# Kernel tuning notes

Hardware: AMD Instinct MI355X
Metric: run time of the kernel (lower is better)

## Reference

```python
import math
import jax, jax.numpy as jnp
import numpy as np

B, N, HID, NH = 4, 1024, 1024, 16
DH = HID // NH
MLP = int(HID * 4.0)


def _ndense(x, w):
    # NormalizedDense: row-normalize kernel (axis=1 for 2D), alpha=sqrt(w[0].size)=sqrt(out),
    # then divide by sqrt(fan_in).
    norm = jnp.linalg.norm(w, axis=1, keepdims=True)
    alpha = jnp.sqrt(jnp.asarray(w.shape[1], x.dtype))
    wn = w / (norm * alpha + 1e-4)
    wn = wn / jnp.sqrt(jnp.asarray(w.shape[0], x.dtype))
    return x @ wn


def mp_silu(x):
    return jax.nn.silu(x) / 0.596


def pixel_norm(x, eps=1e-4):
    return x * jax.lax.rsqrt(jnp.mean(x * x, axis=-1, keepdims=True) + eps)


def mp_add(a, b, t=0.3):
    return ((1 - t) * a + t * b) / math.sqrt((1 - t) ** 2 + t ** 2)


def setup_inputs() -> dict:
    key = jax.random.key(0)
    ks = jax.random.split(key, 9)
    std = 0.02
    return {
        "x": jax.random.normal(ks[0], (B, N, HID), jnp.float32),
        "c": jax.random.normal(ks[1], (B, HID), jnp.float32),
        "w_cond": std * jax.random.normal(ks[2], (HID, 2 * HID), jnp.float32),
        "w_qkv": std * jax.random.normal(ks[3], (HID, 3 * HID), jnp.float32),
        "w_out": std * jax.random.normal(ks[4], (HID, HID), jnp.float32),
        "w_mlp1": std * jax.random.normal(ks[5], (HID, MLP), jnp.float32),
        "w_mlp2": std * jax.random.normal(ks[6], (MLP, HID), jnp.float32),
        "attn_gain": 0.1 * jax.random.normal(ks[7], (), jnp.float32),
        "mlp_gain": 0.1 * jax.random.normal(ks[8], (), jnp.float32),
    }


def reference(x, c, w_cond, w_qkv, w_out, w_mlp1, w_mlp2, attn_gain, mlp_gain):
    # conditioning -> gain/shift
    cc = mp_silu(c)
    cc = _ndense(cc, w_cond)                       # [B, 2H]
    gain, shift = jnp.split(cc, 2, axis=-1)        # [B, H] each

    # attention branch
    x_cond = pixel_norm(x) * (1 + gain[:, None]) + shift[:, None]
    qkv = _ndense(x_cond, w_qkv)                   # [B, N, 3H]
    q, k, v = jnp.split(qkv, 3, axis=-1)
    q, k, v = pixel_norm(q), pixel_norm(k), pixel_norm(v)

    def split_heads(t):
        return t.reshape(B, N, NH, DH).transpose(0, 2, 1, 3)  # [B, NH, N, DH]

    q, k, v = split_heads(q), split_heads(k), split_heads(v)
    q = q / jnp.sqrt(jnp.sum(q * q, axis=-1, keepdims=True) + 1e-6)
    k = k / jnp.sqrt(jnp.sum(k * k, axis=-1, keepdims=True) + 1e-6)

    attn = jnp.einsum('bhnd,bhmd->bhnm', q, k) / math.sqrt(DH)
    attn = jax.nn.softmax(attn, axis=-1)
    x_attn = jnp.einsum('bhnm,bhmd->bhnd', attn, v)
    x_attn = x_attn.transpose(0, 2, 1, 3).reshape(B, N, HID)
    x_attn = pixel_norm(_ndense(x_attn, w_out)) * jnp.exp(attn_gain)
    x = mp_add(x, x_attn, t=0.3)

    # MLP branch
    x_cond = pixel_norm(x) * (1 + gain[:, None]) + shift[:, None]
    h = mp_silu(pixel_norm(_ndense(x_cond, w_mlp1)))
    x_mlp = pixel_norm(_ndense(h, w_mlp2)) * jnp.exp(mlp_gain)
    x = mp_add(x, x_mlp, t=0.3)
    return x
```

## Files before the change

### kernel.cpp

```cpp
#include <hip/hip_runtime.h>

typedef __bf16 bf16_t;
typedef __attribute__((ext_vector_type(8))) __bf16 bh8;
typedef __attribute__((ext_vector_type(4))) __bf16 bh4;
typedef __attribute__((ext_vector_type(4))) float f32x4;

#define DEV static __device__ __forceinline__

typedef __attribute__((address_space(3))) void lds_void;
typedef const __attribute__((address_space(1))) void glb_void;

DEV void async16(const bf16_t* g, bf16_t* l) {
  __builtin_amdgcn_global_load_lds((glb_void*)g, (lds_void*)l, 16, 0, 0);
}

DEV float wave_sum(float v) {
#pragma unroll
  for (int m = 32; m > 0; m >>= 1) v += __shfl_xor(v, m, 64);
  return v;
}

DEV float block_sum(float v, float* sbuf) {
  v = wave_sum(v);
  int wid = threadIdx.x >> 6;
  if ((threadIdx.x & 63) == 0) sbuf[wid] = v;
  __syncthreads();
  float r = sbuf[0] + sbuf[1] + sbuf[2] + sbuf[3];
  __syncthreads();
  return r;
}

__global__ void k_wnorm_all(const float* __restrict__ w_cond, const float* __restrict__ w_qkv,
                            const float* __restrict__ w_out, const float* __restrict__ w_mlp1,
                            const float* __restrict__ w_mlp2, float* __restrict__ s) {
  __shared__ float sbuf[4];
  int id = blockIdx.x;
  const float* W; int N, K, row;
  if (id < 1024)      { W = w_cond; N = 2048; K = 1024; row = id; }
  else if (id < 2048) { W = w_qkv;  N = 3072; K = 1024; row = id - 1024; }
  else if (id < 3072) { W = w_out;  N = 1024; K = 1024; row = id - 2048; }
  else if (id < 4096) { W = w_mlp1; N = 4096; K = 1024; row = id - 3072; }
  else                { W = w_mlp2; N = 1024; K = 4096; row = id - 4096; }
  const float4* wr = (const float4*)(W + (size_t)row * N);
  float acc = 0.f;
  for (int i = threadIdx.x; i < (N >> 2); i += 256) {
    float4 w = wr[i];
    acc += w.x*w.x + w.y*w.y + w.z*w.z + w.w*w.w;
  }
  float tot = block_sum(acc, sbuf);
  if (threadIdx.x == 0) {
    float norm = sqrtf(tot);
    s[id] = 1.0f / ((norm * sqrtf((float)N) + 1e-4f) * sqrtf((float)K));
  }
}

__global__ void k_wtrans_all(const float* __restrict__ w_cond, const float* __restrict__ w_qkv,
                             const float* __restrict__ w_out, const float* __restrict__ w_mlp1,
                             const float* __restrict__ w_mlp2, const float* __restrict__ sall,
                             bf16_t* __restrict__ wt_cond, bf16_t* __restrict__ wt_qkv,
                             bf16_t* __restrict__ wt_out, bf16_t* __restrict__ wt_mlp1,
                             bf16_t* __restrict__ wt_mlp2) {
  __shared__ float tile[64][65];
  int id = blockIdx.x;
  const float* W; const float* s; bf16_t* Wt; int K, N, n0, k0;
  if (id < 512)       { W=w_cond; s=sall;      Wt=wt_cond; K=1024; N=2048; int l=id;      n0=(l&31)*64; k0=(l>>5)*64; }
  else if (id < 1280) { W=w_qkv;  s=sall+1024; Wt=wt_qkv;  K=1024; N=3072; int l=id-512;  n0=(l%48)*64; k0=(l/48)*64; }
  else if (id < 1536) { W=w_out;  s=sall+2048; Wt=wt_out;  K=1024; N=1024; int l=id-1280; n0=(l&15)*64; k0=(l>>4)*64; }
  else if (id < 2560) { W=w_mlp1; s=sall+3072; Wt=wt_mlp1; K=1024; N=4096; int l=id-1536; n0=(l&63)*64; k0=(l>>6)*64; }
  else                { W=w_mlp2; s=sall+4096; Wt=wt_mlp2; K=4096; N=1024; int l=id-2560; n0=(l&15)*64; k0=(l>>4)*64; }
  int tx = threadIdx.x & 63, ty = threadIdx.x >> 6;
  for (int r = ty; r < 64; r += 4)
    tile[r][tx] = W[(size_t)(k0 + r) * N + n0 + tx] * s[k0 + r];
  __syncthreads();
  for (int r = ty; r < 64; r += 4)
    Wt[(size_t)(n0 + r) * K + k0 + tx] = (bf16_t)tile[tx][r];
}

__global__ void k_cond(const float* __restrict__ c, const bf16_t* __restrict__ wt,
                       float* __restrict__ gs) {
  __shared__ float cc[4][1024];
  int t = threadIdx.x;
  for (int i = t; i < 4096; i += 256) {
    int b = i >> 10, col = i & 1023;
    float x = c[b * 1024 + col];
    float sig = 1.f / (1.f + __expf(-x));
    cc[b][col] = x * sig * (1.f / 0.596f);
  }
  __syncthreads();
  int wid = t >> 6, lane = t & 63;
  int j = blockIdx.x * 4 + wid;
  const bf16_t* wr = wt + (size_t)j * 1024;
  float acc0 = 0, acc1 = 0, acc2 = 0, acc3 = 0;
  for (int i = lane; i < 1024; i += 64) {
    float w = (float)wr[i];
    acc0 += cc[0][i] * w; acc1 += cc[1][i] * w;
    acc2 += cc[2][i] * w; acc3 += cc[3][i] * w;
  }
  float v0 = wave_sum(acc0), v1 = wave_sum(acc1), v2 = wave_sum(acc2), v3 = wave_sum(acc3);
  if (lane == 0) {
    gs[0 * 2048 + j] = v0; gs[1 * 2048 + j] = v1;
    gs[2 * 2048 + j] = v2; gs[3 * 2048 + j] = v3;
  }
}

__global__ void k_xcond(const float* __restrict__ x, const float* __restrict__ gs,
                        bf16_t* __restrict__ xc) {
  __shared__ float sbuf[4];
  int row = blockIdx.x, b = row >> 10, t = threadIdx.x;
  float4 v = ((const float4*)(x + (size_t)row * 1024))[t];
  float ss = v.x*v.x + v.y*v.y + v.z*v.z + v.w*v.w;
  float tot = block_sum(ss, sbuf);
  float r = rsqrtf(tot * (1.f/1024.f) + 1e-4f);
  float4 g  = ((const float4*)(gs + b * 2048))[t];
  float4 sh = ((const float4*)(gs + b * 2048 + 1024))[t];
  bh4 o;
  o[0] = (bf16_t)(v.x * r * (1.f + g.x) + sh.x);
  o[1] = (bf16_t)(v.y * r * (1.f + g.y) + sh.y);
  o[2] = (bf16_t)(v.z * r * (1.f + g.z) + sh.z);
  o[3] = (bf16_t)(v.w * r * (1.f + g.w) + sh.w);
  *(bh4*)(xc + (size_t)row * 1024 + t * 4) = o;
}

__global__ __launch_bounds__(256) void k_gemm(const bf16_t* __restrict__ A,
                                              const bf16_t* __restrict__ Bt,
                                              bf16_t* __restrict__ C,
                                              int M, int N, int K, int klen) {
  __shared__ bf16_t As[128][32];
  __shared__ bf16_t Bs[128][32];
  const unsigned gx = gridDim.x;
  const unsigned flat = blockIdx.x + gx * blockIdx.y;
  const unsigned npx = gx >> 3;
  const unsigned xcd = flat & 7, o = flat >> 3;
  const unsigned grp = npx * 8;
  const unsigned mg = o / grp, r = o % grp;
  const int m0 = (mg * 8 + r / npx) * 128;
  const int n0 = (xcd * npx + r % npx) * 128;
  const size_t kbeg = (size_t)blockIdx.z * klen;
  C += (size_t)blockIdx.z * M * N;
  const int t = threadIdx.x, lane = t & 63, wid = t >> 6;
  const int l15 = lane & 15, quad = lane >> 4;
  const int wm = (wid >> 1) * 64, wn = (wid & 1) * 64;
  const int r0 = t >> 2, kc0 = (t & 3) * 8;
  const bf16_t* Ag0 = A + (size_t)(m0 + r0) * K + kbeg + kc0;
  const bf16_t* Ag1 = Ag0 + (size_t)64 * K;
  const bf16_t* Bg0 = Bt + (size_t)(n0 + r0) * K + kbeg + kc0;
  const bf16_t* Bg1 = Bg0 + (size_t)64 * K;
  bf16_t* lA0 = &As[0][0] + wid * 512;
  bf16_t* lB0 = &Bs[0][0] + wid * 512;
  f32x4 acc[4][4] = {};
  for (int k0 = 0; k0 < klen; k0 += 32) {
    async16(Ag0 + k0, lA0);
    async16(Ag1 + k0, lA0 + 2048);
    async16(Bg0 + k0, lB0);
    async16(Bg1 + k0, lB0 + 2048);
    __syncthreads();
    bh8 a[4], bb[4];
#pragma unroll
    for (int i = 0; i < 4; i++) a[i]  = *(const bh8*)&As[wm + i*16 + l15][quad*8];
#pragma unroll
    for (int j = 0; j < 4; j++) bb[j] = *(const bh8*)&Bs[wn + j*16 + l15][quad*8];
#pragma unroll
    for (int i = 0; i < 4; i++)
#pragma unroll
      for (int j = 0; j < 4; j++)
        acc[i][j] = __builtin_amdgcn_mfma_f32_16x16x32_bf16(a[i], bb[j], acc[i][j], 0, 0, 0);
    __syncthreads();
  }
#pragma unroll
  for (int i = 0; i < 4; i++)
#pragma unroll
    for (int j = 0; j < 4; j++)
#pragma unroll
      for (int r2 = 0; r2 < 4; r2++)
        C[(size_t)(m0 + wm + i*16 + quad*4 + r2) * N + n0 + wn + j*16 + l15] =
            (bf16_t)acc[i][j][r2];
}

__global__ void k_qkvnorm(const bf16_t* __restrict__ qkv, bf16_t* __restrict__ qo,
                          bf16_t* __restrict__ ko, bf16_t* __restrict__ vo) {
  __shared__ float sbuf[4];
  const int row = blockIdx.x, b = row >> 10, n = row & 1023, t = threadIdx.x;
  const bf16_t* rp = qkv + (size_t)row * 3072;
  bh4 q4 = *(const bh4*)(rp + t * 4);
  bh4 k4 = *(const bh4*)(rp + 1024 + t * 4);
  bh4 v4 = *(const bh4*)(rp + 2048 + t * 4);
  float4 q = {(float)q4[0], (float)q4[1], (float)q4[2], (float)q4[3]};
  float4 k = {(float)k4[0], (float)k4[1], (float)k4[2], (float)k4[3]};
  float4 v = {(float)v4[0], (float)v4[1], (float)v4[2], (float)v4[3]};
  float sq = q.x*q.x + q.y*q.y + q.z*q.z + q.w*q.w;
  float sk = k.x*k.x + k.y*k.y + k.z*k.z + k.w*k.w;
  float sv = v.x*v.x + v.y*v.y + v.z*v.z + v.w*v.w;
  float tq = block_sum(sq, sbuf);
  float tk = block_sum(sk, sbuf);
  float tv = block_sum(sv, sbuf);
  float rq = rsqrtf(tq * (1.f/1024.f) + 1e-4f);
  float rk = rsqrtf(tk * (1.f/1024.f) + 1e-4f);
  float rv = rsqrtf(tv * (1.f/1024.f) + 1e-4f);
  float hq = sq, hk = sk;
#pragma unroll
  for (int m = 1; m < 16; m <<= 1) { hq += __shfl_xor(hq, m, 64); hk += __shfl_xor(hk, m, 64); }
  float qs = rq * rsqrtf(rq*rq*hq + 1e-6f);
  float ks = rk * rsqrtf(rk*rk*hk + 1e-6f);
  int h = t >> 4, d = (t & 15) * 4;
  size_t base = ((size_t)(b * 16 + h) * 1024 + n) * 64 + d;
  bh4 oq, okk, ov;
  oq[0]=(bf16_t)(q.x*qs); oq[1]=(bf16_t)(q.y*qs); oq[2]=(bf16_t)(q.z*qs); oq[3]=(bf16_t)(q.w*qs);
  okk[0]=(bf16_t)(k.x*ks); okk[1]=(bf16_t)(k.y*ks); okk[2]=(bf16_t)(k.z*ks); okk[3]=(bf16_t)(k.w*ks);
  ov[0]=(bf16_t)(v.x*rv); ov[1]=(bf16_t)(v.y*rv); ov[2]=(bf16_t)(v.z*rv); ov[3]=(bf16_t)(v.w*rv);
  *(bh4*)(qo + base) = oq;
  *(bh4*)(ko + base) = okk;
  *(bh4*)(vo + base) = ov;
}

__global__ __launch_bounds__(256) void k_attn(const bf16_t* __restrict__ Q,
                                              const bf16_t* __restrict__ K,
                                              const bf16_t* __restrict__ V,
                                              bf16_t* __restrict__ O) {
  __shared__ bf16_t Qs[128][72];
  __shared__ bf16_t Ks[64][72];
  __shared__ bf16_t Vt[64][72];
  __shared__ bf16_t Ps[128][72];
  const int qt = blockIdx.x, bh = blockIdx.y;
  const int b = bh >> 4, h = bh & 15;
  const int t = threadIdx.x, lane = t & 63, wid = t >> 6;
  const int l15 = lane & 15, quad = lane >> 4;
  const int strip = wid * 32;
  const bf16_t* Qg = Q + ((size_t)bh * 1024 + qt * 128) * 64;
  const bf16_t* Kg = K + (size_t)bh * 1024 * 64;
  const bf16_t* Vg = V + (size_t)bh * 1024 * 64;
  for (int i = t; i < 1024; i += 256) {
    int r = i >> 3, p = (i & 7) * 8;
    *(bh8*)&Qs[r][p] = *(const bh8*)(Qg + r * 64 + p);
  }
  f32x4 o[2][4] = {};
  float rs[2][4] = {};
  __syncthreads();
  for (int kv0 = 0; kv0 < 1024; kv0 += 64) {
    for (int i = t; i < 512; i += 256) {
      int r = i >> 3, p = (i & 7) * 8;
      *(bh8*)&Ks[r][p] = *(const bh8*)(Kg + (size_t)(kv0 + r) * 64 + p);
      bh8 vv = *(const bh8*)(Vg + (size_t)(kv0 + r) * 64 + p);
#pragma unroll
      for (int j = 0; j < 8; j++) Vt[p + j][r] = vv[j];
    }
    __syncthreads();
    f32x4 s[2][4] = {};
#pragma unroll
    for (int kc = 0; kc < 2; kc++) {
      bh8 aq[2], bk[4];
#pragma unroll
      for (int i = 0; i < 2; i++) aq[i] = *(const bh8*)&Qs[strip + i*16 + l15][kc*32 + quad*8];
#pragma unroll
      for (int j = 0; j < 4; j++) bk[j] = *(const bh8*)&Ks[j*16 + l15][kc*32 + quad*8];
#pragma unroll
      for (int i = 0; i < 2; i++)
#pragma unroll
        for (int j = 0; j < 4; j++)
          s[i][j] = __builtin_amdgcn_mfma_f32_16x16x32_bf16(aq[i], bk[j], s[i][j], 0, 0, 0);
    }
#pragma unroll
    for (int i = 0; i < 2; i++)
#pragma unroll
      for (int j = 0; j < 4; j++)
#pragma unroll
        for (int r = 0; r < 4; r++) {
          float p = __expf(s[i][j][r] * 0.125f);
          bf16_t pb = (bf16_t)p;
          rs[i][r] += (float)pb;
          Ps[strip + i*16 + quad*4 + r][j*16 + l15] = pb;
        }
#pragma unroll
    for (int kc = 0; kc < 2; kc++) {
      bh8 ap[2], bv[4];
#pragma unroll
      for (int i = 0; i < 2; i++) ap[i] = *(const bh8*)&Ps[strip + i*16 + l15][kc*32 + quad*8];
#pragma unroll
      for (int j = 0; j < 4; j++) bv[j] = *(const bh8*)&Vt[j*16 + l15][kc*32 + quad*8];
#pragma unroll
      for (int i = 0; i < 2; i++)
#pragma unroll
        for (int j = 0; j < 4; j++)
          o[i][j] = __builtin_amdgcn_mfma_f32_16x16x32_bf16(ap[i], bv[j], o[i][j], 0, 0, 0);
    }
    __syncthreads();
  }
#pragma unroll
  for (int i = 0; i < 2; i++)
#pragma unroll
    for (int r = 0; r < 4; r++) {
      float v = rs[i][r];
      v += __shfl_xor(v, 1, 64); v += __shfl_xor(v, 2, 64);
      v += __shfl_xor(v, 4, 64); v += __shfl_xor(v, 8, 64);
      float inv = 1.f / v;
      int n = qt * 128 + strip + i*16 + quad*4 + r;
#pragma unroll
      for (int j = 0; j < 4; j++)
        O[((size_t)b * 1024 + n) * 1024 + h*64 + j*16 + l15] = (bf16_t)(o[i][j][r] * inv);
    }
}

__global__ void k_amerge(const bf16_t* __restrict__ y, const float* __restrict__ x,
                         const float* __restrict__ gs, const float* __restrict__ again,
                         bf16_t* __restrict__ x1, bf16_t* __restrict__ xc2) {
  __shared__ float sbuf[4];
  int row = blockIdx.x, b = row >> 10, t = threadIdx.x;
  const size_t PS = (size_t)4096 * 1024;
  bh4 a0 = *(const bh4*)(y + (size_t)row * 1024 + t * 4);
  bh4 a1 = *(const bh4*)(y + PS + (size_t)row * 1024 + t * 4);
  float4 yv;
  yv.x = (float)a0[0] + (float)a1[0]; yv.y = (float)a0[1] + (float)a1[1];
  yv.z = (float)a0[2] + (float)a1[2]; yv.w = (float)a0[3] + (float)a1[3];
  float4 xv = ((const float4*)(x + (size_t)row * 1024))[t];
  float ss = yv.x*yv.x + yv.y*yv.y + yv.z*yv.z + yv.w*yv.w;
  float tot = block_sum(ss, sbuf);
  float r = rsqrtf(tot * (1.f/1024.f) + 1e-4f);
  float ag = __expf(again[0]);
  const float C1 = 0.7f / 0.76157731059f, C2 = 0.3f / 0.76157731059f;
  float4 xo;
  xo.x = C1 * xv.x + C2 * (yv.x * r * ag);
  xo.y = C1 * xv.y + C2 * (yv.y * r * ag);
  xo.z = C1 * xv.z + C2 * (yv.z * r * ag);
  xo.w = C1 * xv.w + C2 * (yv.w * r * ag);
  bh4 x1o;
  x1o[0] = (bf16_t)xo.x; x1o[1] = (bf16_t)xo.y; x1o[2] = (bf16_t)xo.z; x1o[3] = (bf16_t)xo.w;
  *(bh4*)(x1 + (size_t)row * 1024 + t * 4) = x1o;
  float ss1 = xo.x*xo.x + xo.y*xo.y + xo.z*xo.z + xo.w*xo.w;
  float tot1 = block_sum(ss1, sbuf);
  float r1 = rsqrtf(tot1 * (1.f/1024.f) + 1e-4f);
  float4 g  = ((const float4*)(gs + b * 2048))[t];
  float4 sh = ((const float4*)(gs + b * 2048 + 1024))[t];
  bh4 o;
  o[0] = (bf16_t)(xo.x * r1 * (1.f + g.x) + sh.x);
  o[1] = (bf16_t)(xo.y * r1 * (1.f + g.y) + sh.y);
  o[2] = (bf16_t)(xo.z * r1 * (1.f + g.z) + sh.z);
  o[3] = (bf16_t)(xo.w * r1 * (1.f + g.w) + sh.w);
  *(bh4*)(xc2 + (size_t)row * 1024 + t * 4) = o;
}

__global__ void k_mlpnorm(const bf16_t* __restrict__ hf, bf16_t* __restrict__ hb) {
  __shared__ float sbuf[4];
  int row = blockIdx.x, t = threadIdx.x;
  const bf16_t* rp = hf + (size_t)row * 4096;
  float4 v[4]; float ss = 0.f;
#pragma unroll
  for (int i = 0; i < 4; i++) {
    bh4 bv = *(const bh4*)(rp + (t + 256 * i) * 4);
    v[i].x = (float)bv[0]; v[i].y = (float)bv[1]; v[i].z = (float)bv[2]; v[i].w = (float)bv[3];
    ss += v[i].x*v[i].x + v[i].y*v[i].y + v[i].z*v[i].z + v[i].w*v[i].w;
  }
  float tot = block_sum(ss, sbuf);
  float r = rsqrtf(tot * (1.f/4096.f) + 1e-4f);
#pragma unroll
  for (int i = 0; i < 4; i++) {
    float a[4] = {v[i].x, v[i].y, v[i].z, v[i].w};
    bh4 o;
#pragma unroll
    for (int j = 0; j < 4; j++) {
      float u = a[j] * r;
      float sig = 1.f / (1.f + __expf(-u));
      o[j] = (bf16_t)(u * sig * (1.f / 0.596f));
    }
    *(bh4*)(hb + (size_t)row * 4096 + (t + 256 * i) * 4) = o;
  }
}

__global__ void k_fmerge(const bf16_t* __restrict__ y, const bf16_t* __restrict__ x1,
                         const float* __restrict__ mgain, float* __restrict__ out) {
  __shared__ float sbuf[4];
  int row = blockIdx.x, t = threadIdx.x;
  const size_t PS = (size_t)4096 * 1024;
  float4 yv = {0.f, 0.f, 0.f, 0.f};
#pragma unroll
  for (int p = 0; p < 4; p++) {
    bh4 yp = *(const bh4*)(y + p * PS + (size_t)row * 1024 + t * 4);
    yv.x += (float)yp[0]; yv.y += (float)yp[1]; yv.z += (float)yp[2]; yv.w += (float)yp[3];
  }
  bh4 xb = *(const bh4*)(x1 + (size_t)row * 1024 + t * 4);
  float4 xv = {(float)xb[0], (float)xb[1], (float)xb[2], (float)xb[3]};
  float ss = yv.x*yv.x + yv.y*yv.y + yv.z*yv.z + yv.w*yv.w;
  float tot = block_sum(ss, sbuf);
  float r = rsqrtf(tot * (1.f/1024.f) + 1e-4f);
  float mg = __expf(mgain[0]);
  const float C1 = 0.7f / 0.76157731059f, C2 = 0.3f / 0.76157731059f;
  float4 o;
  o.x = C1 * xv.x + C2 * (yv.x * r * mg);
  o.y = C1 * xv.y + C2 * (yv.y * r * mg);
  o.z = C1 * xv.z + C2 * (yv.z * r * mg);
  o.w = C1 * xv.w + C2 * (yv.w * r * mg);
  ((float4*)(out + (size_t)row * 1024))[t] = o;
}

extern "C" void kernel_launch(void* const* d_in, const int* in_sizes, int n_in,
                              void* d_out, int out_size, void* d_ws, size_t ws_size,
                              hipStream_t stream) {
  const float* x      = (const float*)d_in[0];
  const float* c      = (const float*)d_in[1];
  const float* w_cond = (const float*)d_in[2];
  const float* w_qkv  = (const float*)d_in[3];
  const float* w_out  = (const float*)d_in[4];
  const float* w_mlp1 = (const float*)d_in[5];
  const float* w_mlp2 = (const float*)d_in[6];
  const float* again  = (const float*)d_in[7];
  const float* mgain  = (const float*)d_in[8];
  float* out = (float*)d_out;
  char* ws = (char*)d_ws;

  bf16_t* wt_cond = (bf16_t*)(ws + 0);
  bf16_t* wt_qkv  = (bf16_t*)(ws + 4194304);
  bf16_t* wt_out  = (bf16_t*)(ws + 10485760);
  bf16_t* wt_mlp1 = (bf16_t*)(ws + 12582912);
  bf16_t* wt_mlp2 = (bf16_t*)(ws + 20971520);
  float*  sn      = (float*)(ws + 29360128);
  float*  gs      = (float*)(ws + 29392896);
  bf16_t* xc      = (bf16_t*)(ws + 29425664);
  bf16_t* qh      = (bf16_t*)(ws + 37814272);
  bf16_t* kh      = (bf16_t*)(ws + 46202880);
  bf16_t* vh      = (bf16_t*)(ws + 54591488);
  bf16_t* xattn   = (bf16_t*)(ws + 62980096);
  bf16_t* hb      = (bf16_t*)(ws + 37814272);
  bf16_t* x1      = (bf16_t*)(ws + 71368704);
  bf16_t* buf_b   = (bf16_t*)(ws + 88145920);

  k_wnorm_all<<<8192, 256, 0, stream>>>(w_cond, w_qkv, w_out, w_mlp1, w_mlp2, sn);
  k_wtrans_all<<<3584, 256, 0, stream>>>(w_cond, w_qkv, w_out, w_mlp1, w_mlp2, sn,
                                         wt_cond, wt_qkv, wt_out, wt_mlp1, wt_mlp2);

  k_cond<<<512, 256, 0, stream>>>(c, wt_cond, gs);
  k_xcond<<<4096, 256, 0, stream>>>(x, gs, xc);
  k_gemm<<<dim3(24, 32, 1), 256, 0, stream>>>(xc, wt_qkv, buf_b, 4096, 3072, 1024, 1024);
  k_qkvnorm<<<4096, 256, 0, stream>>>(buf_b, qh, kh, vh);
  k_attn<<<dim3(8, 64), 256, 0, stream>>>(qh, kh, vh, xattn);
  k_gemm<<<dim3(8, 32, 2), 256, 0, stream>>>(xattn, wt_out, buf_b, 4096, 1024, 1024, 512);
  k_amerge<<<4096, 256, 0, stream>>>(buf_b, x, gs, again, x1, xc);
  k_gemm<<<dim3(32, 32, 1), 256, 0, stream>>>(xc, wt_mlp1, buf_b, 4096, 4096, 1024, 1024);
  k_mlpnorm<<<4096, 256, 0, stream>>>(buf_b, hb);
  k_gemm<<<dim3(8, 32, 4), 256, 0, stream>>>(hb, wt_mlp2, buf_b, 4096, 1024, 4096, 1024);
  k_fmerge<<<4096, 256, 0, stream>>>(buf_b, x1, mgain, out);
  (void)in_sizes; (void)n_in; (void)out_size; (void)ws_size;
}
```

Baseline: 426.0 us.

## Deepen GEMM K-step, shrink attention query tile, halve MLP2 split-K

The GEMM kernel now stages two 32-wide K slices per loop iteration, doubling LDS tiles so each barrier pair covers twice the MFMA work. The attention kernel moves from 128-row to 64-row query tiles, with each wave owning 16 rows, which doubles the grid to fill more CUs. The MLP down-projection split-K drops from 4 to 2 partitions, and the final merge reads fewer partial buffers. Together these aim to cut barrier overhead, raise attention occupancy and reduce partial-sum traffic, at the cost of more K/V reloads in attention and less parallelism in the last GEMM.

```diff
diff --git a/kernel.cpp b/kernel.cpp
--- a/kernel.cpp
+++ b/kernel.cpp
@@ -125,16 +125,16 @@
                                               const bf16_t* __restrict__ Bt,
                                               bf16_t* __restrict__ C,
                                               int M, int N, int K, int klen) {
-  __shared__ bf16_t As[128][32];
-  __shared__ bf16_t Bs[128][32];
+  __shared__ bf16_t As[2][128][32];
+  __shared__ bf16_t Bs[2][128][32];
   const unsigned gx = gridDim.x;
   const unsigned flat = blockIdx.x + gx * blockIdx.y;
   const unsigned npx = gx >> 3;
   const unsigned xcd = flat & 7, o = flat >> 3;
   const unsigned grp = npx * 8;
-  const unsigned mg = o / grp, r = o % grp;
-  const int m0 = (mg * 8 + r / npx) * 128;
-  const int n0 = (xcd * npx + r % npx) * 128;
+  const unsigned mg = o / grp, rr = o % grp;
+  const int m0 = (mg * 8 + rr / npx) * 128;
+  const int n0 = (xcd * npx + rr % npx) * 128;
   const size_t kbeg = (size_t)blockIdx.z * klen;
   C += (size_t)blockIdx.z * M * N;
   const int t = threadIdx.x, lane = t & 63, wid = t >> 6;
@@ -142,28 +142,32 @@
   const int wm = (wid >> 1) * 64, wn = (wid & 1) * 64;
   const int r0 = t >> 2, kc0 = (t & 3) * 8;
   const bf16_t* Ag0 = A + (size_t)(m0 + r0) * K + kbeg + kc0;
-  const bf16_t* Ag1 = Ag0 + (size_t)64 * K;
   const bf16_t* Bg0 = Bt + (size_t)(n0 + r0) * K + kbeg + kc0;
-  const bf16_t* Bg1 = Bg0 + (size_t)64 * K;
-  bf16_t* lA0 = &As[0][0] + wid * 512;
-  bf16_t* lB0 = &Bs[0][0] + wid * 512;
+  bf16_t* lA0 = &As[0][0][0] + wid * 512;
+  bf16_t* lB0 = &Bs[0][0][0] + wid * 512;
   f32x4 acc[4][4] = {};
-  for (int k0 = 0; k0 < klen; k0 += 32) {
-    async16(Ag0 + k0, lA0);
-    async16(Ag1 + k0, lA0 + 2048);
-    async16(Bg0 + k0, lB0);
-    async16(Bg1 + k0, lB0 + 2048);
+  for (int k0 = 0; k0 < klen; k0 += 64) {
+#pragma unroll
+    for (int h = 0; h < 2; h++) {
+      async16(Ag0 + k0 + h * 32, lA0 + h * 4096);
+      async16(Ag0 + k0 + h * 32 + (size_t)64 * K, lA0 + h * 4096 + 2048);
+      async16(Bg0 + k0 + h * 32, lB0 + h * 4096);
+      async16(Bg0 + k0 + h * 32 + (size_t)64 * K, lB0 + h * 4096 + 2048);
+    }
     __syncthreads();
-    bh8 a[4], bb[4];
-#pragma unroll
-    for (int i = 0; i < 4; i++) a[i]  = *(const bh8*)&As[wm + i*16 + l15][quad*8];
-#pragma unroll
-    for (int j = 0; j < 4; j++) bb[j] = *(const bh8*)&Bs[wn + j*16 + l15][quad*8];
-#pragma unroll
-    for (int i = 0; i < 4; i++)
-#pragma unroll
-      for (int j = 0; j < 4; j++)
-        acc[i][j] = __builtin_amdgcn_mfma_f32_16x16x32_bf16(a[i], bb[j], acc[i][j], 0, 0, 0);
+#pragma unroll
+    for (int h = 0; h < 2; h++) {
+      bh8 a[4], bb[4];
+#pragma unroll
+      for (int i = 0; i < 4; i++) a[i]  = *(const bh8*)&As[h][wm + i*16 + l15][quad*8];
+#pragma unroll
+      for (int j = 0; j < 4; j++) bb[j] = *(const bh8*)&Bs[h][wn + j*16 + l15][quad*8];
+#pragma unroll
+      for (int i = 0; i < 4; i++)
+#pragma unroll
+        for (int j = 0; j < 4; j++)
+          acc[i][j] = __builtin_amdgcn_mfma_f32_16x16x32_bf16(a[i], bb[j], acc[i][j], 0, 0, 0);
+    }
     __syncthreads();
   }
 #pragma unroll
@@ -216,24 +220,24 @@
                                               const bf16_t* __restrict__ K,
                                               const bf16_t* __restrict__ V,
                                               bf16_t* __restrict__ O) {
-  __shared__ bf16_t Qs[128][72];
+  __shared__ bf16_t Qs[64][72];
   __shared__ bf16_t Ks[64][72];
   __shared__ bf16_t Vt[64][72];
-  __shared__ bf16_t Ps[128][72];
+  __shared__ bf16_t Ps[64][72];
   const int qt = blockIdx.x, bh = blockIdx.y;
   const int b = bh >> 4, h = bh & 15;
   const int t = threadIdx.x, lane = t & 63, wid = t >> 6;
   const int l15 = lane & 15, quad = lane >> 4;
-  const int strip = wid * 32;
-  const bf16_t* Qg = Q + ((size_t)bh * 1024 + qt * 128) * 64;
+  const int strip = wid * 16;
+  const bf16_t* Qg = Q + ((size_t)bh * 1024 + qt * 64) * 64;
   const bf16_t* Kg = K + (size_t)bh * 1024 * 64;
   const bf16_t* Vg = V + (size_t)bh * 1024 * 64;
-  for (int i = t; i < 1024; i += 256) {
+  for (int i = t; i < 512; i += 256) {
     int r = i >> 3, p = (i & 7) * 8;
     *(bh8*)&Qs[r][p] = *(const bh8*)(Qg + r * 64 + p);
   }
-  f32x4 o[2][4] = {};
-  float rs[2][4] = {};
+  f32x4 o[4] = {};
+  float rs[4] = {};
   __syncthreads();
   for (int kv0 = 0; kv0 < 1024; kv0 += 64) {
     for (int i = t; i < 512; i += 256) {
@@ -244,59 +248,49 @@
       for (int j = 0; j < 8; j++) Vt[p + j][r] = vv[j];
     }
     __syncthreads();
-    f32x4 s[2][4] = {};
+    f32x4 s[4] = {};
 #pragma unroll
     for (int kc = 0; kc < 2; kc++) {
-      bh8 aq[2], bk[4];
-#pragma unroll
-      for (int i = 0; i < 2; i++) aq[i] = *(const bh8*)&Qs[strip + i*16 + l15][kc*32 + quad*8];
+      bh8 aq = *(const bh8*)&Qs[strip + l15][kc*32 + quad*8];
+      bh8 bk[4];
 #pragma unroll
       for (int j = 0; j < 4; j++) bk[j] = *(const bh8*)&Ks[j*16 + l15][kc*32 + quad*8];
 #pragma unroll
-      for (int i = 0; i < 2; i++)
-#pragma unroll
-        for (int j = 0; j < 4; j++)
-          s[i][j] = __builtin_amdgcn_mfma_f32_16x16x32_bf16(aq[i], bk[j], s[i][j], 0, 0, 0);
-    }
-#pragma unroll
-    for (int i = 0; i < 2; i++)
-#pragma unroll
       for (int j = 0; j < 4; j++)
-#pragma unroll
-        for (int r = 0; r < 4; r++) {
-          float p = __expf(s[i][j][r] * 0.125f);
-          bf16_t pb = (bf16_t)p;
-          rs[i][r] += (float)pb;
-          Ps[strip + i*16 + quad*4 + r][j*16 + l15] = pb;
-        }
+        s[j] = __builtin_amdgcn_mfma_f32_16x16x32_bf16(aq, bk[j], s[j], 0, 0, 0);
+    }
+#pragma unroll
+    for (int j = 0; j < 4; j++)
+#pragma unroll
+      for (int r = 0; r < 4; r++) {
+        float p = __expf(s[j][r] * 0.125f);
+        bf16_t pb = (bf16_t)p;
+        rs[r] += (float)pb;
+        Ps[strip + quad*4 + r][j*16 + l15] = pb;
+      }
 #pragma unroll
     for (int kc = 0; kc < 2; kc++) {
-      bh8 ap[2], bv[4];
-#pragma unroll
-      for (int i = 0; i < 2; i++) ap[i] = *(const bh8*)&Ps[strip + i*16 + l15][kc*32 + quad*8];
+      bh8 ap = *(const bh8*)&Ps[strip + l15][kc*32 + quad*8];
+      bh8 bv[4];
 #pragma unroll
       for (int j = 0; j < 4; j++) bv[j] = *(const bh8*)&Vt[j*16 + l15][kc*32 + quad*8];
 #pragma unroll
-      for (int i = 0; i < 2; i++)
-#pragma unroll
-        for (int j = 0; j < 4; j++)
-          o[i][j] = __builtin_amdgcn_mfma_f32_16x16x32_bf16(ap[i], bv[j], o[i][j], 0, 0, 0);
+      for (int j = 0; j < 4; j++)
+        o[j] = __builtin_amdgcn_mfma_f32_16x16x32_bf16(ap, bv[j], o[j], 0, 0, 0);
     }
     __syncthreads();
   }
 #pragma unroll
-  for (int i = 0; i < 2; i++)
-#pragma unroll
-    for (int r = 0; r < 4; r++) {
-      float v = rs[i][r];
-      v += __shfl_xor(v, 1, 64); v += __shfl_xor(v, 2, 64);
-      v += __shfl_xor(v, 4, 64); v += __shfl_xor(v, 8, 64);
-      float inv = 1.f / v;
-      int n = qt * 128 + strip + i*16 + quad*4 + r;
-#pragma unroll
-      for (int j = 0; j < 4; j++)
-        O[((size_t)b * 1024 + n) * 1024 + h*64 + j*16 + l15] = (bf16_t)(o[i][j][r] * inv);
-    }
+  for (int r = 0; r < 4; r++) {
+    float v = rs[r];
+    v += __shfl_xor(v, 1, 64); v += __shfl_xor(v, 2, 64);
+    v += __shfl_xor(v, 4, 64); v += __shfl_xor(v, 8, 64);
+    float inv = 1.f / v;
+    int n = qt * 64 + strip + quad*4 + r;
+#pragma unroll
+    for (int j = 0; j < 4; j++)
+      O[((size_t)b * 1024 + n) * 1024 + h*64 + j*16 + l15] = (bf16_t)(o[j][r] * inv);
+  }
 }
 
 __global__ void k_amerge(const bf16_t* __restrict__ y, const float* __restrict__ x,
@@ -371,7 +365,7 @@
   const size_t PS = (size_t)4096 * 1024;
   float4 yv = {0.f, 0.f, 0.f, 0.f};
 #pragma unroll
-  for (int p = 0; p < 4; p++) {
+  for (int p = 0; p < 2; p++) {
     bh4 yp = *(const bh4*)(y + p * PS + (size_t)row * 1024 + t * 4);
     yv.x += (float)yp[0]; yv.y += (float)yp[1]; yv.z += (float)yp[2]; yv.w += (float)yp[3];
   }
@@ -429,12 +423,12 @@
   k_xcond<<<4096, 256, 0, stream>>>(x, gs, xc);
   k_gemm<<<dim3(24, 32, 1), 256, 0, stream>>>(xc, wt_qkv, buf_b, 4096, 3072, 1024, 1024);
   k_qkvnorm<<<4096, 256, 0, stream>>>(buf_b, qh, kh, vh);
-  k_attn<<<dim3(8, 64), 256, 0, stream>>>(qh, kh, vh, xattn);
+  k_attn<<<dim3(16, 64), 256, 0, stream>>>(qh, kh, vh, xattn);
   k_gemm<<<dim3(8, 32, 2), 256, 0, stream>>>(xattn, wt_out, buf_b, 4096, 1024, 1024, 512);
   k_amerge<<<4096, 256, 0, stream>>>(buf_b, x, gs, again, x1, xc);
   k_gemm<<<dim3(32, 32, 1), 256, 0, stream>>>(xc, wt_mlp1, buf_b, 4096, 4096, 1024, 1024);
   k_mlpnorm<<<4096, 256, 0, stream>>>(buf_b, hb);
-  k_gemm<<<dim3(8, 32, 4), 256, 0, stream>>>(hb, wt_mlp2, buf_b, 4096, 1024, 4096, 1024);
+  k_gemm<<<dim3(8, 32, 2), 256, 0, stream>>>(hb, wt_mlp2, buf_b, 4096, 1024, 4096, 2048);
   k_fmerge<<<4096, 256, 0, stream>>>(buf_b, x1, mgain, out);
   (void)in_sizes; (void)n_in; (void)out_size; (void)ws_size;
 }
```

Result: faster. 402.1 us (-5.6%).
